# Kernel optimization log

Hardware: AMD Instinct MI355X
Metric: run time of the kernel (lower is better)

The kernel has to match this reference:

```python
import jax, jax.numpy as jnp
import numpy as np
import math

WINDOW_SIZE = 11
SIGMA = 1.5
C3 = 0.0001


def _make_window(window_size=WINDOW_SIZE, sigma=SIGMA):
    # 1D gaussian, normalized, then outer product -> [1,1,K,K] (OIHW)
    xs = np.arange(window_size, dtype=np.float64)
    g = np.exp(-((xs - window_size // 2) ** 2) / (2.0 * sigma ** 2))
    g = g / g.sum()
    w2d = np.outer(g, g).astype(np.float32)
    return jnp.asarray(w2d)[None, None, :, :]


def setup_inputs() -> dict:
    key = jax.random.key(0)
    k1, k2 = jax.random.split(key)
    B, C, H, W = 32, 1, 512, 512
    input1 = jax.random.normal(k1, (B, C, H, W), dtype=jnp.float32)
    input2 = jax.random.normal(k2, (B, C, H, W), dtype=jnp.float32)
    window = _make_window()
    return {"input1": input1, "input2": input2, "window": window}


def _conv_valid(x, window):
    # x: [N,1,H,W], window: [1,1,K,K], channel=1 so groups=1 is exact
    return jax.lax.conv_general_dilated(
        x, window, window_strides=(1, 1), padding="VALID",
        dimension_numbers=("NCHW", "OIHW", "NCHW"))


def reference(input1, input2, window):
    B = input1.shape[0]
    # Fuse the five gaussian box-filters into one conv over a stacked batch
    stacked = jnp.concatenate(
        [input1, input2, input1 * input1, input2 * input2, input1 * input2],
        axis=0)  # [5B,1,H,W]
    filt = _conv_valid(stacked, window)  # [5B,1,H',W']
    mu1, mu2, e11, e22, e12 = (filt[i * B:(i + 1) * B] for i in range(5))
    sigma1_sq = e11 - mu1 * mu1
    sigma2_sq = e22 - mu2 * mu2
    sigma12 = e12 - mu1 * mu2
    s = (sigma12 + C3) / (jnp.sqrt(jnp.abs(sigma1_sq)) * jnp.sqrt(jnp.abs(sigma2_sq)) + C3)
    return jnp.mean(s)
```

## Files before the change

### kernel.cpp

```cpp
#include <hip/hip_runtime.h>
#include <math.h>

#define KW 11
#define HALO 10
#define TY 32
#define BATCH 32
#define HH 512
#define WW 512
#define OH 502
#define OW 502
#define NSX 8
#define WPB 2
#define NBX 4
#define NBY 16
#define NWAVE (BATCH * NBY * NSX)
#define C3V 1.0e-4f
#define SW 80

typedef float v2f __attribute__((ext_vector_type(2)));

static __device__ __forceinline__ float rfl(float x) {
    return __int_as_float(__builtin_amdgcn_readfirstlane(__float_as_int(x)));
}

__global__ __launch_bounds__(128) void ssim_strip_kernel(
    const float* __restrict__ in1,
    const float* __restrict__ in2,
    const float* __restrict__ win,
    double* __restrict__ partials)
{
    __shared__ v2f sh[WPB][KW][SW];

    const int t = threadIdx.x;
    const int wid = t >> 6;
    const int lane = t & 63;
    const int strip = blockIdx.x * WPB + wid;
    const int x0 = strip * 64;
    const int y0 = blockIdx.y * TY;
    const int img = blockIdx.z;

    const int nx = min(64, OW - x0);
    const int ny = min(TY, OH - y0);

    v2f gp[6];
    {
        const float c = sqrtf(win[5 * KW + 5]);
        #pragma unroll
        for (int i = 0; i < 6; ++i) {
            const float w = rfl(win[i * KW + 5] / c);
            gp[i] = (v2f){w, w};
        }
    }
    #define GW(j) gp[(j) <= 5 ? (j) : 10 - (j)]

    const float maskf = (lane < nx) ? 1.f : 0.f;
    const bool stager = lane < 40;
    const int scol = min(x0 + 2 * lane, WW - 2);
    const float* b1 = in1 + (size_t)img * HH * WW;
    const float* b2 = in2 + (size_t)img * HH * WW;

    v2f* const mysh = &sh[wid][0][0];

    v2f va, vb;
#define LOADR(q) { const int rq = min(y0 + (q), HH - 1);             \
    va = *(const v2f*)(b1 + (size_t)rq * WW + scol);                 \
    vb = *(const v2f*)(b2 + (size_t)rq * WW + scol); }
#define WRITES(slot) { if (stager)                                    \
    *(float4*)&mysh[(slot) * SW + 2 * lane] =                         \
        make_float4(va.x, vb.x, va.y, vb.y); }
#define RDWIN(slot) { _Pragma("unroll")                               \
    for (int j = 0; j < KW; ++j) W[j] = mysh[(slot) * SW + lane + j]; }

    v2f accab[KW], accsq[KW];
    float acc4[KW];
    #pragma unroll
    for (int i = 0; i < KW; ++i) {
        accab[i] = (v2f){0.f, 0.f}; accsq[i] = (v2f){0.f, 0.f}; acc4[i] = 0.f;
    }

    v2f W[KW];
    double tsum = 0.0;

    LOADR(0);
    WRITES(0);
    RDWIN(0);
    LOADR(1);

    for (int c = 0; c < 4; ++c) {
        float csum = 0.f;
        #pragma unroll
        for (int p = 0; p < KW; ++p) {
            const int yr = c * KW + p;

            v2f hab = (v2f){0.f, 0.f}, hsq = (v2f){0.f, 0.f};
            float h4 = 0.f;
            #pragma unroll
            for (int j = 0; j < KW; ++j) {
                const v2f ab = W[j];
                const v2f g = GW(j);
                const v2f gab = g * ab;
                hab = __builtin_elementwise_fma(g, ab, hab);
                hsq = __builtin_elementwise_fma(gab, ab, hsq);
                h4 = fmaf(gab.x, ab.y, h4);
            }

            WRITES((p + 1) % KW);
            RDWIN((p + 1) % KW);
            LOADR(yr + 2);

            #pragma unroll
            for (int r = 0; r < KW; ++r) {
                const int j = (r - p + KW) % KW;
                const v2f g = GW(10 - j);
                if (j == 10) {
                    accab[r] = g * hab;
                    accsq[r] = g * hsq;
                    acc4[r] = g.x * h4;
                } else {
                    accab[r] = __builtin_elementwise_fma(g, hab, accab[r]);
                    accsq[r] = __builtin_elementwise_fma(g, hsq, accsq[r]);
                    acc4[r] = fmaf(g.x, h4, acc4[r]);
                }
            }
            if (yr >= HALO) {
                const v2f mu = accab[p];
                const v2f sq = __builtin_elementwise_fma(-mu, mu, accsq[p]);
                const float s12 = fmaf(-mu.x, mu.y, acc4[p]);
                const float den = __builtin_amdgcn_sqrtf(fabsf(sq.x * sq.y)) + C3V;
                const float s = (s12 + C3V) * __builtin_amdgcn_rcpf(den);
                const float m = ((yr - HALO) < ny) ? maskf : 0.f;
                csum = fmaf(s, m, csum);
            }
        }
        tsum += (double)csum;
    }
#undef LOADR
#undef WRITES
#undef RDWIN
#undef GW

    #pragma unroll
    for (int off = 32; off > 0; off >>= 1)
        tsum += __shfl_down(tsum, off, 64);
    if (lane == 0) {
        const int bid = (img * NBY + blockIdx.y) * NSX + strip;
        partials[bid] = tsum;
    }
}

__global__ __launch_bounds__(256) void ssim_reduce_kernel(
    const double* __restrict__ partials, float* __restrict__ out)
{
    __shared__ double sred[4];
    double s = 0.0;
    for (int i = threadIdx.x; i < NWAVE; i += 256) s += partials[i];
    #pragma unroll
    for (int off = 32; off > 0; off >>= 1)
        s += __shfl_down(s, off, 64);
    const int wid = threadIdx.x >> 6;
    const int lane = threadIdx.x & 63;
    if (lane == 0) sred[wid] = s;
    __syncthreads();
    if (threadIdx.x == 0) {
        const double total = sred[0] + sred[1] + sred[2] + sred[3];
        out[0] = (float)(total / ((double)BATCH * OH * OW));
    }
}

extern "C" void kernel_launch(void* const* d_in, const int* in_sizes, int n_in,
                              void* d_out, int out_size, void* d_ws, size_t ws_size,
                              hipStream_t stream) {
    const float* in1 = (const float*)d_in[0];
    const float* in2 = (const float*)d_in[1];
    const float* win = (const float*)d_in[2];
    float* out = (float*)d_out;
    double* partials = (double*)d_ws;

    dim3 grid(NBX, NBY, BATCH);
    dim3 block(WPB * 64);
    ssim_strip_kernel<<<grid, block, 0, stream>>>(in1, in2, win, partials);
    ssim_reduce_kernel<<<1, 256, 0, stream>>>(partials, out);
}
```

Measured before the change: 48.22 us.

## Double-buffer LDS window reads and pin instruction schedule with sched_group_barrier

Splits the register window into two alternating buffers so the next row's LDS reads are issued before the current row's horizontal convolution. Staging runs one row further ahead, and every lane now writes without the lane<40 guard into a widened 128-entry stride. The main loop is unrolled over 22 rows with explicit sched_group_barrier groups that interleave LDS reads, VALU work, the LDS write and global loads. The halo branch becomes an unsigned mask comparison. This is meant to hide LDS latency, but it raises register pressure and doubles LDS footprint.

```diff
diff --git a/kernel.cpp b/kernel.cpp
--- a/kernel.cpp
+++ b/kernel.cpp
@@ -15,7 +15,7 @@
 #define NBY 16
 #define NWAVE (BATCH * NBY * NSX)
 #define C3V 1.0e-4f
-#define SW 80
+#define SW 128
 
 typedef float v2f __attribute__((ext_vector_type(2)));
 
@@ -29,7 +29,7 @@
     const float* __restrict__ win,
     double* __restrict__ partials)
 {
-    __shared__ v2f sh[WPB][KW][SW];
+    __shared__ v2f sh[WPB][KW * SW];
 
     const int t = threadIdx.x;
     const int wid = t >> 6;
@@ -54,22 +54,31 @@
     #define GW(j) gp[(j) <= 5 ? (j) : 10 - (j)]
 
     const float maskf = (lane < nx) ? 1.f : 0.f;
-    const bool stager = lane < 40;
     const int scol = min(x0 + 2 * lane, WW - 2);
     const float* b1 = in1 + (size_t)img * HH * WW;
     const float* b2 = in2 + (size_t)img * HH * WW;
 
-    v2f* const mysh = &sh[wid][0][0];
+    v2f* const mysh = &sh[wid][0];
 
-    v2f va, vb;
-#define LOADR(q) { const int rq = min(y0 + (q), HH - 1);             \
-    va = *(const v2f*)(b1 + (size_t)rq * WW + scol);                 \
-    vb = *(const v2f*)(b2 + (size_t)rq * WW + scol); }
-#define WRITES(slot) { if (stager)                                    \
-    *(float4*)&mysh[(slot) * SW + 2 * lane] =                         \
-        make_float4(va.x, vb.x, va.y, vb.y); }
-#define RDWIN(slot) { _Pragma("unroll")                               \
-    for (int j = 0; j < KW; ++j) W[j] = mysh[(slot) * SW + lane + j]; }
+    v2f sva, svb;
+    v2f W0[KW], W1[KW];
+
+#define LOADR(q) { const int rq = min(y0 + (q), HH - 1);               \
+    sva = *(const v2f*)(b1 + (size_t)rq * WW + scol);                  \
+    svb = *(const v2f*)(b2 + (size_t)rq * WW + scol); }
+#define WRITES(slot) {                                                  \
+    *(float4*)&mysh[(slot) * SW + 2 * lane] =                           \
+        make_float4(sva.x, svb.x, sva.y, svb.y); }
+#define RDWIN(slot, Warr) { const v2f* rp = mysh + (slot) * SW + lane;  \
+    _Pragma("unroll") for (int j = 0; j < KW; ++j) Warr[j] = rp[j]; }
+#define HCONV(Warr) {                                                   \
+    _Pragma("unroll") for (int j = 0; j < KW; ++j) {                    \
+        const v2f ab = Warr[j];                                         \
+        const v2f g = GW(j);                                            \
+        const v2f gab = g * ab;                                         \
+        hab = __builtin_elementwise_fma(g, ab, hab);                    \
+        hsq = __builtin_elementwise_fma(gab, ab, hsq);                  \
+        h4 = fmaf(gab.x, ab.y, h4); } }
 
     v2f accab[KW], accsq[KW];
     float acc4[KW];
@@ -78,39 +87,39 @@
         accab[i] = (v2f){0.f, 0.f}; accsq[i] = (v2f){0.f, 0.f}; acc4[i] = 0.f;
     }
 
-    v2f W[KW];
     double tsum = 0.0;
 
-    LOADR(0);
-    WRITES(0);
-    RDWIN(0);
-    LOADR(1);
+    LOADR(0); WRITES(0);
+    LOADR(1); WRITES(1);
+    RDWIN(0, W0);
+    LOADR(2);
 
-    for (int c = 0; c < 4; ++c) {
+    for (int c = 0; c < 2; ++c) {
+        const int cbase = c * 22;
         float csum = 0.f;
         #pragma unroll
-        for (int p = 0; p < KW; ++p) {
-            const int yr = c * KW + p;
+        for (int p = 0; p < 22; ++p) {
+            const int pe = p % KW;
+            const int yr = cbase + p;
+
+            if ((p & 1) == 0) { RDWIN((pe + 1) % KW, W1); }
+            else              { RDWIN((pe + 1) % KW, W0); }
+            __builtin_amdgcn_sched_group_barrier(0x100, 11, 0);
 
             v2f hab = (v2f){0.f, 0.f}, hsq = (v2f){0.f, 0.f};
             float h4 = 0.f;
-            #pragma unroll
-            for (int j = 0; j < KW; ++j) {
-                const v2f ab = W[j];
-                const v2f g = GW(j);
-                const v2f gab = g * ab;
-                hab = __builtin_elementwise_fma(g, ab, hab);
-                hsq = __builtin_elementwise_fma(gab, ab, hsq);
-                h4 = fmaf(gab.x, ab.y, h4);
-            }
+            if ((p & 1) == 0) { HCONV(W0); } else { HCONV(W1); }
+            __builtin_amdgcn_sched_group_barrier(0x2, 40, 0);
 
-            WRITES((p + 1) % KW);
-            RDWIN((p + 1) % KW);
-            LOADR(yr + 2);
+            WRITES((pe + 2) % KW);
+            __builtin_amdgcn_sched_group_barrier(0x200, 1, 0);
+
+            LOADR(yr + 3);
+            __builtin_amdgcn_sched_group_barrier(0x20, 2, 0);
 
             #pragma unroll
             for (int r = 0; r < KW; ++r) {
-                const int j = (r - p + KW) % KW;
+                const int j = (r - pe + KW) % KW;
                 const v2f g = GW(10 - j);
                 if (j == 10) {
                     accab[r] = g * hab;
@@ -122,21 +131,20 @@
                     acc4[r] = fmaf(g.x, h4, acc4[r]);
                 }
             }
-            if (yr >= HALO) {
-                const v2f mu = accab[p];
-                const v2f sq = __builtin_elementwise_fma(-mu, mu, accsq[p]);
-                const float s12 = fmaf(-mu.x, mu.y, acc4[p]);
-                const float den = __builtin_amdgcn_sqrtf(fabsf(sq.x * sq.y)) + C3V;
-                const float s = (s12 + C3V) * __builtin_amdgcn_rcpf(den);
-                const float m = ((yr - HALO) < ny) ? maskf : 0.f;
-                csum = fmaf(s, m, csum);
-            }
+            const v2f mu = accab[pe];
+            const v2f sq = __builtin_elementwise_fma(-mu, mu, accsq[pe]);
+            const float s12 = fmaf(-mu.x, mu.y, acc4[pe]);
+            const float den = __builtin_amdgcn_sqrtf(fabsf(sq.x * sq.y)) + C3V;
+            const float s = (s12 + C3V) * __builtin_amdgcn_rcpf(den);
+            const float m = ((unsigned)(yr - HALO) < (unsigned)ny) ? maskf : 0.f;
+            csum = fmaf(s, m, csum);
         }
         tsum += (double)csum;
     }
 #undef LOADR
 #undef WRITES
 #undef RDWIN
+#undef HCONV
 #undef GW
 
     #pragma unroll
```

After: 54.40 us. +12.8%, slower.

## Compute two output columns per lane with 128-wide strips per wavefront

Applied to the files above, without the earlier changes.

Each lane now produces two adjacent output columns, so every wavefront covers a 128-column strip and the horizontal pass reads a 12-wide window with vectorized float4 LDS loads shared by both columns. Rows past the valid tile are skipped, and the row mask check is hoisted. This cuts per-output LDS traffic and the halo overhead per strip, and it halves the number of blocks. In exchange it roughly doubles accumulator registers, which may lower occupancy or cause spills, and it leaves fewer blocks to spread across CUs.

```diff
diff --git a/kernel.cpp b/kernel.cpp
--- a/kernel.cpp
+++ b/kernel.cpp
@@ -9,13 +9,14 @@
 #define WW 512
 #define OH 502
 #define OW 502
-#define NSX 8
+#define SPW 128
+#define NSX 4
 #define WPB 2
-#define NBX 4
+#define NBX 2
 #define NBY 16
 #define NWAVE (BATCH * NBY * NSX)
 #define C3V 1.0e-4f
-#define SW 80
+#define SW 144
 
 typedef float v2f __attribute__((ext_vector_type(2)));
 
@@ -35,12 +36,12 @@
     const int wid = t >> 6;
     const int lane = t & 63;
     const int strip = blockIdx.x * WPB + wid;
-    const int x0 = strip * 64;
+    const int x0 = strip * SPW;
     const int y0 = blockIdx.y * TY;
     const int img = blockIdx.z;
 
-    const int nx = min(64, OW - x0);
     const int ny = min(TY, OH - y0);
+    const int rows = ny + HALO;
 
     v2f gp[6];
     {
@@ -53,86 +54,111 @@
     }
     #define GW(j) gp[(j) <= 5 ? (j) : 10 - (j)]
 
-    const float maskf = (lane < nx) ? 1.f : 0.f;
-    const bool stager = lane < 40;
-    const int scol = min(x0 + 2 * lane, WW - 2);
+    const int cA = x0 + 2 * lane;
+    const v2f mcol = (v2f){ cA < OW ? 1.f : 0.f, (cA + 1) < OW ? 1.f : 0.f };
+
     const float* b1 = in1 + (size_t)img * HH * WW;
     const float* b2 = in2 + (size_t)img * HH * WW;
+    const int hc = min(x0 + SPW + 2 * lane, WW - 2);
+    const bool hstage = lane < 5;
 
     v2f* const mysh = &sh[wid][0][0];
 
-    v2f va, vb;
-#define LOADR(q) { const int rq = min(y0 + (q), HH - 1);             \
-    va = *(const v2f*)(b1 + (size_t)rq * WW + scol);                 \
-    vb = *(const v2f*)(b2 + (size_t)rq * WW + scol); }
-#define WRITES(slot) { if (stager)                                    \
-    *(float4*)&mysh[(slot) * SW + 2 * lane] =                         \
-        make_float4(va.x, vb.x, va.y, vb.y); }
-#define RDWIN(slot) { _Pragma("unroll")                               \
-    for (int j = 0; j < KW; ++j) W[j] = mysh[(slot) * SW + lane + j]; }
-
-    v2f accab[KW], accsq[KW];
-    float acc4[KW];
+    v2f va, vb, ha, hb;
+#define LOADR(q) { const int rq = min(y0 + (q), HH - 1);                  \
+    const float* r1 = b1 + (size_t)rq * WW;                               \
+    const float* r2 = b2 + (size_t)rq * WW;                               \
+    va = *(const v2f*)(r1 + cA); vb = *(const v2f*)(r2 + cA);             \
+    if (hstage) { ha = *(const v2f*)(r1 + hc); hb = *(const v2f*)(r2 + hc); } }
+#define WRITES(slot) {                                                     \
+    *(float4*)&mysh[(slot) * SW + 2 * lane] =                              \
+        make_float4(va.x, vb.x, va.y, vb.y);                               \
+    if (hstage) *(float4*)&mysh[(slot) * SW + SPW + 2 * lane] =            \
+        make_float4(ha.x, hb.x, ha.y, hb.y); }
+
+    v2f W[12];
+#define RDWIN(slot) { const v2f* rp = mysh + (slot) * SW + 2 * lane;       \
+    _Pragma("unroll") for (int j = 0; j < 6; ++j)                          \
+        *(float4*)&W[2 * j] = *(const float4*)&rp[2 * j]; }
+
+    v2f aabA[KW], asqA[KW], aabB[KW], asqB[KW];
+    float a4A[KW], a4B[KW];
     #pragma unroll
     for (int i = 0; i < KW; ++i) {
-        accab[i] = (v2f){0.f, 0.f}; accsq[i] = (v2f){0.f, 0.f}; acc4[i] = 0.f;
-    }
-
-    v2f W[KW];
+        aabA[i] = (v2f){0.f, 0.f}; asqA[i] = (v2f){0.f, 0.f}; a4A[i] = 0.f;
+        aabB[i] = (v2f){0.f, 0.f}; asqB[i] = (v2f){0.f, 0.f}; a4B[i] = 0.f;
+    }
+
     double tsum = 0.0;
 
     LOADR(0);
     WRITES(0);
-    RDWIN(0);
     LOADR(1);
 
     for (int c = 0; c < 4; ++c) {
-        float csum = 0.f;
+        v2f csum = (v2f){0.f, 0.f};
         #pragma unroll
         for (int p = 0; p < KW; ++p) {
             const int yr = c * KW + p;
-
-            v2f hab = (v2f){0.f, 0.f}, hsq = (v2f){0.f, 0.f};
-            float h4 = 0.f;
-            #pragma unroll
-            for (int j = 0; j < KW; ++j) {
-                const v2f ab = W[j];
-                const v2f g = GW(j);
-                const v2f gab = g * ab;
-                hab = __builtin_elementwise_fma(g, ab, hab);
-                hsq = __builtin_elementwise_fma(gab, ab, hsq);
-                h4 = fmaf(gab.x, ab.y, h4);
-            }
-
-            WRITES((p + 1) % KW);
-            RDWIN((p + 1) % KW);
-            LOADR(yr + 2);
-
-            #pragma unroll
-            for (int r = 0; r < KW; ++r) {
-                const int j = (r - p + KW) % KW;
-                const v2f g = GW(10 - j);
-                if (j == 10) {
-                    accab[r] = g * hab;
-                    accsq[r] = g * hsq;
-                    acc4[r] = g.x * h4;
-                } else {
-                    accab[r] = __builtin_elementwise_fma(g, hab, accab[r]);
-                    accsq[r] = __builtin_elementwise_fma(g, hsq, accsq[r]);
-                    acc4[r] = fmaf(g.x, h4, acc4[r]);
+            if (yr < rows) {
+                RDWIN(p);
+                WRITES((p + 1) % KW);
+                LOADR(yr + 2);
+
+                v2f habA = (v2f){0.f, 0.f}, hsqA = (v2f){0.f, 0.f};
+                v2f habB = (v2f){0.f, 0.f}, hsqB = (v2f){0.f, 0.f};
+                float h4A = 0.f, h4B = 0.f;
+                #pragma unroll
+                for (int j = 0; j < 12; ++j) {
+                    const v2f ab = W[j];
+                    const v2f sq = ab * ab;
+                    const float p4 = ab.x * ab.y;
+                    if (j < 11) {
+                        const v2f g = GW(j);
+                        habA = __builtin_elementwise_fma(g, ab, habA);
+                        hsqA = __builtin_elementwise_fma(g, sq, hsqA);
+                        h4A = fmaf(g.x, p4, h4A);
+                    }
+                    if (j > 0) {
+                        const v2f g = GW(j - 1);
+                        habB = __builtin_elementwise_fma(g, ab, habB);
+                        hsqB = __builtin_elementwise_fma(g, sq, hsqB);
+                        h4B = fmaf(g.x, p4, h4B);
+                    }
+                }
+
+                #pragma unroll
+                for (int r = 0; r < KW; ++r) {
+                    const int j = (r - p + KW) % KW;
+                    const v2f g = GW(10 - j);
+                    if (j == 10) {
+                        aabA[r] = g * habA; asqA[r] = g * hsqA; a4A[r] = g.x * h4A;
+                        aabB[r] = g * habB; asqB[r] = g * hsqB; a4B[r] = g.x * h4B;
+                    } else {
+                        aabA[r] = __builtin_elementwise_fma(g, habA, aabA[r]);
+                        asqA[r] = __builtin_elementwise_fma(g, hsqA, asqA[r]);
+                        a4A[r] = fmaf(g.x, h4A, a4A[r]);
+                        aabB[r] = __builtin_elementwise_fma(g, habB, aabB[r]);
+                        asqB[r] = __builtin_elementwise_fma(g, hsqB, asqB[r]);
+                        a4B[r] = fmaf(g.x, h4B, a4B[r]);
+                    }
+                }
+
+                if (yr >= HALO && (yr - HALO) < ny) {
+                    const v2f muA = aabA[p], muB = aabB[p];
+                    const v2f sqA = __builtin_elementwise_fma(-muA, muA, asqA[p]);
+                    const v2f sqB = __builtin_elementwise_fma(-muB, muB, asqB[p]);
+                    const float s12A = fmaf(-muA.x, muA.y, a4A[p]);
+                    const float s12B = fmaf(-muB.x, muB.y, a4B[p]);
+                    const float dA = __builtin_amdgcn_sqrtf(fabsf(sqA.x * sqA.y)) + C3V;
+                    const float dB = __builtin_amdgcn_sqrtf(fabsf(sqB.x * sqB.y)) + C3V;
+                    const v2f s2 = (v2f){ (s12A + C3V) * __builtin_amdgcn_rcpf(dA),
+                                          (s12B + C3V) * __builtin_amdgcn_rcpf(dB) };
+                    csum = __builtin_elementwise_fma(s2, mcol, csum);
                 }
             }
-            if (yr >= HALO) {
-                const v2f mu = accab[p];
-                const v2f sq = __builtin_elementwise_fma(-mu, mu, accsq[p]);
-                const float s12 = fmaf(-mu.x, mu.y, acc4[p]);
-                const float den = __builtin_amdgcn_sqrtf(fabsf(sq.x * sq.y)) + C3V;
-                const float s = (s12 + C3V) * __builtin_amdgcn_rcpf(den);
-                const float m = ((yr - HALO) < ny) ? maskf : 0.f;
-                csum = fmaf(s, m, csum);
-            }
         }
-        tsum += (double)csum;
+        tsum += (double)csum.x + (double)csum.y;
     }
 #undef LOADR
 #undef WRITES
```

Result: no change. 48.91 us (+1.4%).

## Software-pipeline row loads two deep and skew horizontal pass by one row

Applied to the files above, without the earlier changes.

Restructures the per-row loop so global loads are issued two rows ahead using alternating register sets. The horizontal filter for the next row is computed after the vertical accumulation of the current row, which hides LDS read latency behind arithmetic. An early-exit guard skips rows past the valid range. The change adds register pressure from the extra buffers and a per-phase branch, and the A/B swap across chunks with an odd phase count makes the logic subtle.

```diff
diff --git a/kernel.cpp b/kernel.cpp
--- a/kernel.cpp
+++ b/kernel.cpp
@@ -41,6 +41,7 @@
 
     const int nx = min(64, OW - x0);
     const int ny = min(TY, OH - y0);
+    const int rows = ny + HALO;
 
     v2f gp[6];
     {
@@ -61,15 +62,24 @@
 
     v2f* const mysh = &sh[wid][0][0];
 
-    v2f va, vb;
-#define LOADR(q) { const int rq = min(y0 + (q), HH - 1);             \
-    va = *(const v2f*)(b1 + (size_t)rq * WW + scol);                 \
-    vb = *(const v2f*)(b2 + (size_t)rq * WW + scol); }
-#define WRITES(slot) { if (stager)                                    \
-    *(float4*)&mysh[(slot) * SW + 2 * lane] =                         \
-        make_float4(va.x, vb.x, va.y, vb.y); }
-#define RDWIN(slot) { _Pragma("unroll")                               \
-    for (int j = 0; j < KW; ++j) W[j] = mysh[(slot) * SW + lane + j]; }
+    v2f vaA, vbA, vaB, vbB;
+
+#define LOADR_A(q) { const int rq = min(y0 + (q), HH - 1);            \
+    vaA = *(const v2f*)(b1 + (size_t)rq * WW + scol);                 \
+    vbA = *(const v2f*)(b2 + (size_t)rq * WW + scol); }
+#define LOADR_B(q) { const int rq = min(y0 + (q), HH - 1);            \
+    vaB = *(const v2f*)(b1 + (size_t)rq * WW + scol);                 \
+    vbB = *(const v2f*)(b2 + (size_t)rq * WW + scol); }
+#define WRITES_A(slot) { if (stager)                                   \
+    *(float4*)&mysh[(slot) * SW + 2 * lane] =                          \
+        make_float4(vaA.x, vbA.x, vaA.y, vbA.y); }
+#define WRITES_B(slot) { if (stager)                                   \
+    *(float4*)&mysh[(slot) * SW + 2 * lane] =                          \
+        make_float4(vaB.x, vbB.x, vaB.y, vbB.y); }
+
+    v2f W[KW];
+#define RDWIN(slot) { const v2f* rp = mysh + (slot) * SW + lane;       \
+    _Pragma("unroll") for (int j = 0; j < KW; ++j) W[j] = rp[j]; }
 
     v2f accab[KW], accsq[KW];
     float acc4[KW];
@@ -78,64 +88,85 @@
         accab[i] = (v2f){0.f, 0.f}; accsq[i] = (v2f){0.f, 0.f}; acc4[i] = 0.f;
     }
 
-    v2f W[KW];
+    v2f hab = (v2f){0.f, 0.f}, hsq = (v2f){0.f, 0.f};
+    float h4 = 0.f;
+
     double tsum = 0.0;
 
-    LOADR(0);
-    WRITES(0);
+    LOADR_A(0); WRITES_A(0);
+    LOADR_B(1);
+    LOADR_A(2);
     RDWIN(0);
-    LOADR(1);
+
+#define PHASE(p, SET) {                                                 \
+    const int yr = cbase + (p);                                         \
+    if (yr <= rows) {                                                   \
+                      \
+        WRITES_##SET(((p) + 1) % KW);                                   \
+                             \
+        LOADR_##SET(yr + 3);                                            \
+              \
+        {                                                               \
+            const int pe = ((p) + 10) % KW;                             \
+            _Pragma("unroll")                                           \
+            for (int r = 0; r < KW; ++r) {                              \
+                const int j = (r - pe + KW) % KW;                       \
+                const v2f g = GW(10 - j);                               \
+                if (j == 10) {                                          \
+                    accab[r] = g * hab; accsq[r] = g * hsq;             \
+                    acc4[r] = g.x * h4;                                 \
+                } else {                                                \
+                    accab[r] = __builtin_elementwise_fma(g, hab, accab[r]); \
+                    accsq[r] = __builtin_elementwise_fma(g, hsq, accsq[r]); \
+                    acc4[r] = fmaf(g.x, h4, acc4[r]);                   \
+                }                                                       \
+            }                                                           \
+                  \
+            const int yrv = yr - 1;                                     \
+            const v2f mu = accab[pe];                                   \
+            const v2f sq = __builtin_elementwise_fma(-mu, mu, accsq[pe]); \
+            const float s12 = fmaf(-mu.x, mu.y, acc4[pe]);              \
+            const float den = __builtin_amdgcn_sqrtf(fabsf(sq.x * sq.y)) + C3V; \
+            const float s = (s12 + C3V) * __builtin_amdgcn_rcpf(den);   \
+            const float m = ((unsigned)(yrv - HALO) < (unsigned)ny) ? maskf : 0.f; \
+            csum = fmaf(s, m, csum);                                    \
+        }                                                               \
+                      \
+        {                                                               \
+            v2f nab = (v2f){0.f, 0.f}, nsq = (v2f){0.f, 0.f};           \
+            float n4 = 0.f;                                             \
+            _Pragma("unroll")                                           \
+            for (int j = 0; j < KW; ++j) {                              \
+                const v2f ab = W[j];                                    \
+                const v2f g = GW(j);                                    \
+                const v2f gab = g * ab;                                 \
+                nab = __builtin_elementwise_fma(g, ab, nab);            \
+                nsq = __builtin_elementwise_fma(gab, ab, nsq);          \
+                n4 = fmaf(gab.x, ab.y, n4);                             \
+            }                                                           \
+            hab = nab; hsq = nsq; h4 = n4;                              \
+        }                                                               \
+         \
+        RDWIN(((p) + 1) % KW);                                          \
+    }                                                                   \
+}
 
     for (int c = 0; c < 4; ++c) {
+        const int cbase = c * KW;
         float csum = 0.f;
-        #pragma unroll
-        for (int p = 0; p < KW; ++p) {
-            const int yr = c * KW + p;
-
-            v2f hab = (v2f){0.f, 0.f}, hsq = (v2f){0.f, 0.f};
-            float h4 = 0.f;
-            #pragma unroll
-            for (int j = 0; j < KW; ++j) {
-                const v2f ab = W[j];
-                const v2f g = GW(j);
-                const v2f gab = g * ab;
-                hab = __builtin_elementwise_fma(g, ab, hab);
-                hsq = __builtin_elementwise_fma(gab, ab, hsq);
-                h4 = fmaf(gab.x, ab.y, h4);
-            }
-
-            WRITES((p + 1) % KW);
-            RDWIN((p + 1) % KW);
-            LOADR(yr + 2);
-
-            #pragma unroll
-            for (int r = 0; r < KW; ++r) {
-                const int j = (r - p + KW) % KW;
-                const v2f g = GW(10 - j);
-                if (j == 10) {
-                    accab[r] = g * hab;
-                    accsq[r] = g * hsq;
-                    acc4[r] = g.x * h4;
-                } else {
-                    accab[r] = __builtin_elementwise_fma(g, hab, accab[r]);
-                    accsq[r] = __builtin_elementwise_fma(g, hsq, accsq[r]);
-                    acc4[r] = fmaf(g.x, h4, acc4[r]);
-                }
-            }
-            if (yr >= HALO) {
-                const v2f mu = accab[p];
-                const v2f sq = __builtin_elementwise_fma(-mu, mu, accsq[p]);
-                const float s12 = fmaf(-mu.x, mu.y, acc4[p]);
-                const float den = __builtin_amdgcn_sqrtf(fabsf(sq.x * sq.y)) + C3V;
-                const float s = (s12 + C3V) * __builtin_amdgcn_rcpf(den);
-                const float m = ((yr - HALO) < ny) ? maskf : 0.f;
-                csum = fmaf(s, m, csum);
-            }
-        }
+        PHASE(0, B) PHASE(1, A) PHASE(2, B) PHASE(3, A) PHASE(4, B)
+        PHASE(5, A) PHASE(6, B) PHASE(7, A) PHASE(8, B) PHASE(9, A)
+        PHASE(10, B)
         tsum += (double)csum;
-    }
-#undef LOADR
-#undef WRITES
+        { v2f tmp;
+          tmp = vaA; vaA = vaB; vaB = tmp;
+          tmp = vbA; vbA = vbB; vbB = tmp; }
+    }
+#undef PHASE
+#undef LOADR_A
+#undef LOADR_B
+#undef WRITES_A
+#undef WRITES_B
 #undef RDWIN
 #undef GW
 
```

Result: slower. 61.22 us (+27.0%).
